# Performance work log

Measured on AMD Instinct MI355X. Metric: run time of the kernel, lower is better.

## Reference

```python
import jax, jax.numpy as jnp
import numpy as np

NF = 64      # feature channels of h
K = 3        # dynamic filter spatial size (padding=1 in source implies k=3)
FACTOR = 4   # pixel-unshuffle factor


def shuffle_down(x, f):
    # torch pixel_unshuffle: (B,C,H*f,W*f) -> (B,C*f*f,H,W)
    B, C, H, W = x.shape
    x = x.reshape(B, C, H // f, f, W // f, f)
    x = x.transpose(0, 1, 3, 5, 2, 4)
    return x.reshape(B, C * f * f, H // f, W // f)


def _patches3x3(x):
    # x: (B,C,H,W) -> (B,C,9,H,W): zero-padded 3x3 neighborhoods, row-major taps,
    # identical to the identity-filter grouped conv (im2col) in the source.
    H, W = x.shape[-2], x.shape[-1]
    xp = jnp.pad(x, ((0, 0), (0, 0), (1, 1), (1, 1)))
    shifts = [xp[:, :, dy:dy + H, dx:dx + W] for dy in range(K) for dx in range(K)]
    return jnp.stack(shifts, axis=2)


def setup_inputs() -> dict:
    key = jax.random.key(0)
    k1, k2, k3, k4 = jax.random.split(key, 4)
    B, H, W = 2, 256, 256
    h = jax.random.normal(k1, (B, NF, H, W), dtype=jnp.float32)
    i_t = jax.random.normal(k2, (B, 3, H * FACTOR, W * FACTOR), dtype=jnp.float32)
    conv_w = jax.random.normal(k3, (K * K, 3 * FACTOR ** 2, K, K), dtype=jnp.float32) * 0.05
    conv_b = jax.random.normal(k4, (K * K,), dtype=jnp.float32) * 0.05
    return {"h": h, "i_t": i_t, "conv_w": conv_w, "conv_b": conv_b}


def reference(h, i_t, conv_w, conv_b):
    # predict per-pixel 3x3 filters from the shuffled-down guidance frame
    x = shuffle_down(i_t, FACTOR)  # (B, 48, H, W)
    f = jax.lax.conv_general_dilated(
        x, conv_w, window_strides=(1, 1), padding=((1, 1), (1, 1)),
        dimension_numbers=("NCHW", "OIHW", "NCHW"))
    filters = jax.nn.relu(f + conv_b[None, :, None, None])  # (B, 9, H, W)

    # dynamic per-pixel conv: same 3x3 filter applied to every channel of h
    patches = _patches3x3(h)  # (B, nf, 9, H, W)
    out = jnp.einsum("bcfhw,bfhw->bchw", patches, filters)  # (B, nf, H, W)
    return out
```

## Files before the change

### kernel.cpp

```cpp
#include <hip/hip_runtime.h>

#define HSZ 256
#define WSZ 256
#define NFC 64
#define PLANE (HSZ * WSZ)

typedef __attribute__((ext_vector_type(8))) short short8;
typedef __attribute__((ext_vector_type(4))) float f32x4;

__device__ inline unsigned short f2bf(float f) {
    unsigned u = __builtin_bit_cast(unsigned, f);
    return (unsigned short)((u + 0x7fffu + ((u >> 16) & 1u)) >> 16);
}

__global__ __launch_bounds__(512, 4) void fused_dynfilter_v6(
    const float* __restrict__ hbuf,
    const float* __restrict__ i_t,
    const float* __restrict__ wbuf,
    const float* __restrict__ bias,
    float* __restrict__ out)
{
    __shared__ __align__(16) unsigned char smem[41856];
    unsigned short* const xs  = (unsigned short*)smem;
    unsigned short* const lwT = (unsigned short*)(smem + 32640);
    float* const lf = (float*)(smem + 32640);

    const int tid = threadIdx.x;

    const int lin = blockIdx.x + 8 * (blockIdx.y + 32 * blockIdx.z);
    const int q   = ((int)gridDim.z * 256) >> 3;
    const int nid = (lin & 7) * q + (lin >> 3);
    const int b   = nid >> 8;
    const int rem = nid & 255;
    const int X0  = (rem & 7) * 32;
    const int Y0  = (rem >> 3) * 8;

    const int lane = tid & 63;
    const int l15  = lane & 15;
    const int kg   = lane >> 4;
    const int wv   = tid >> 6;
    const int xh   = wv & 1;
    const int r0   = (wv >> 1) * 2;

    const float bv = (l15 < 9) ? bias[l15] : 0.f;
    const float* itb = i_t + (size_t)b * 3 * (PLANE * 16);

    {
        float4 lreg[8]; int sdst[8];
#pragma unroll
        for (int k = 0; k < 8; ++k) {
            const int v = tid + 512 * k;
            const int sp = v / 12, t = v - sp * 12;
            const int c3 = t >> 2, fy = t & 3;
            const int ly = sp / 34, lx = sp - ly * 34;
            const int Y = Y0 - 1 + ly, X = X0 - 1 + lx;
            float4 val = make_float4(0.f, 0.f, 0.f, 0.f);
            if (v < 4080 && (unsigned)Y < HSZ && (unsigned)X < WSZ)
                val = *(const float4*)(itb + ((size_t)c3 * 1024 + (4 * Y + fy)) * 1024 + 4 * X);
            lreg[k] = val;
            sdst[k] = (v < 4080) ? (sp * 48 + t * 4) : -1;
        }
#pragma unroll
        for (int k = 0; k < 8; ++k)
            if (sdst[k] >= 0) {
                ushort4 u{f2bf(lreg[k].x), f2bf(lreg[k].y), f2bf(lreg[k].z), f2bf(lreg[k].w)};
                *(ushort4*)(xs + sdst[k]) = u;
            }
    }

    {
        float4 wr[2];
#pragma unroll
        for (int k = 0; k < 2; ++k) {
            const int v = tid + 512 * k;
            wr[k] = (v < 972) ? *(const float4*)(wbuf + (size_t)v * 4)
                              : make_float4(0.f, 0.f, 0.f, 0.f);
        }
#pragma unroll
        for (int k = 0; k < 2; ++k) {
            const int v = tid + 512 * k;
            if (v < 972) {
                const float e[4] = {wr[k].x, wr[k].y, wr[k].z, wr[k].w};
#pragma unroll
                for (int j = 0; j < 4; ++j) {
                    const int n  = v * 4 + j;
                    const int oc = n / 432;
                    const int r  = n - 432 * oc;
                    const int ic = r / 9;
                    const int kk = r - 9 * ic;
                    lwT[oc * 432 + kk * 48 + ic] = f2bf(e[j]);
                }
            }
        }
    }

    __syncthreads();

    short8 wf[14];
    {
        const unsigned short* lwb = lwT + l15 * 432 + kg * 8;
#pragma unroll
        for (int kb = 0; kb < 14; ++kb) {
            short8 w = {0, 0, 0, 0, 0, 0, 0, 0};
            if (l15 < 9 && !(kb == 13 && kg >= 2))
                w = *(const short8*)(lwb + kb * 32);
            wf[kb] = w;
        }
    }

    f32x4 acc0 = {0.f, 0.f, 0.f, 0.f}, acc1 = acc0;
#pragma unroll
    for (int kb = 0; kb < 14; ++kb) {
        const int k0 = kb * 32 + kg * 8;
        int off = 0;
        if (k0 < 432) {
            const int kk = k0 / 48, ic0 = k0 - 48 * kk;
            const int ky = kk / 3, kx = kk - 3 * ky;
            off = ((r0 + ky) * 34 + 16 * xh + l15 + kx) * 48 + ic0;
        }
        short8 a0 = *(const short8*)(xs + off);
        short8 a1 = *(const short8*)(xs + off + 1632);
        acc0 = __builtin_amdgcn_mfma_f32_16x16x32_bf16(a0, wf[kb], acc0, 0, 0, 0);
        acc1 = __builtin_amdgcn_mfma_f32_16x16x32_bf16(a1, wf[kb], acc1, 0, 0, 0);
    }

    __syncthreads();

    const int pq  = tid & 7;
    const int py  = (tid >> 3) & 7;
    const int clo = tid >> 6;
    const int col0 = X0 + pq * 4;
    const bool gl = (col0 >= 4);
    const bool gr = (col0 <= WSZ - 8);

    bool rg[3]; int ro[3];
#pragma unroll
    for (int ky = 0; ky < 3; ++ky) {
        const int Y = Y0 + py - 1 + ky;
        rg[ky] = ((unsigned)Y < HSZ);
        ro[ky] = Y * WSZ + col0;
    }
    const float* hp = hbuf + ((size_t)b * NFC + clo * 8) * PLANE;

    float4 pf[9];
#pragma unroll
    for (int ky = 0; ky < 3; ++ky) {
        pf[ky * 3 + 0] = (rg[ky] && gl) ? *(const float4*)(hp + ro[ky] - 4)
                                        : make_float4(0.f, 0.f, 0.f, 0.f);
        pf[ky * 3 + 1] = rg[ky] ? *(const float4*)(hp + ro[ky])
                                : make_float4(0.f, 0.f, 0.f, 0.f);
        pf[ky * 3 + 2] = (rg[ky] && gr) ? *(const float4*)(hp + ro[ky] + 4)
                                        : make_float4(0.f, 0.f, 0.f, 0.f);
    }

    if (l15 < 9) {
#pragma unroll
        for (int t = 0; t < 2; ++t) {
            const int pyw = r0 + t;
            const f32x4 A = t ? acc1 : acc0;
#pragma unroll
            for (int r = 0; r < 4; ++r)
                lf[l15 * 256 + pyw * 32 + 16 * xh + kg * 4 + r] = fmaxf(A[r] + bv, 0.f);
        }
    }

    __syncthreads();

    float4 flt[9];
#pragma unroll
    for (int oc = 0; oc < 9; ++oc)
        flt[oc] = *(const float4*)(lf + oc * 256 + py * 32 + pq * 4);

    float* op = out + ((size_t)b * NFC + clo * 8) * PLANE
                    + (size_t)(Y0 + py) * WSZ + col0;

#pragma unroll
    for (int it = 0; it < 8; ++it) {
        const float* p = hp + (size_t)it * PLANE;

        float a[4] = {0.f, 0.f, 0.f, 0.f};
#pragma unroll
        for (int ky = 0; ky < 3; ++ky) {
            float4 lv, mv, rv;
            if (it == 0) {
                lv = pf[ky * 3 + 0]; mv = pf[ky * 3 + 1]; rv = pf[ky * 3 + 2];
            } else {
                lv = (rg[ky] && gl) ? *(const float4*)(p + ro[ky] - 4)
                                    : make_float4(0.f, 0.f, 0.f, 0.f);
                mv = rg[ky] ? *(const float4*)(p + ro[ky])
                            : make_float4(0.f, 0.f, 0.f, 0.f);
                rv = (rg[ky] && gr) ? *(const float4*)(p + ro[ky] + 4)
                                    : make_float4(0.f, 0.f, 0.f, 0.f);
            }
            const float vs[12] = {lv.x, lv.y, lv.z, lv.w,
                                  mv.x, mv.y, mv.z, mv.w,
                                  rv.x, rv.y, rv.z, rv.w};
#pragma unroll
            for (int kx = 0; kx < 3; ++kx)
#pragma unroll
                for (int j = 0; j < 4; ++j)
                    a[j] = fmaf(vs[3 + kx + j], flt[ky * 3 + kx][j], a[j]);
        }

        *(float4*)(op + (size_t)it * PLANE)
            = make_float4(a[0], a[1], a[2], a[3]);
    }
}

extern "C" void kernel_launch(void* const* d_in, const int* in_sizes, int n_in,
                              void* d_out, int out_size, void* d_ws, size_t ws_size,
                              hipStream_t stream) {
    const float* h      = (const float*)d_in[0];
    const float* i_t    = (const float*)d_in[1];
    const float* conv_w = (const float*)d_in[2];
    const float* conv_b = (const float*)d_in[3];
    float* out = (float*)d_out;

    const int B = in_sizes[0] / (NFC * PLANE);
    dim3 grid(8, 32, B);
    fused_dynfilter_v6<<<grid, 512, 0, stream>>>(h, i_t, conv_w, conv_b, out);
}
```

Before: 120.1 us.

## Double tile height, share horizontal halo via lane shuffles, prefetch next channel

Blocks grow to 1024 threads covering 16x32 output tiles, which halves the redundant guidance halo rows loaded per tile. In the dynamic-filter stage each thread now loads only its own float4 of h plus single edge scalars, and gets the left and right neighbours through wavefront shuffles instead of three float4 loads per row. The next channel's h values are software-prefetched into registers while the current one is computed, and one barrier is removed. Tradeoffs: about 85KB of LDS and 1024-thread blocks limit how many blocks fit per CU, and the extra shuffles and register pressure may cut occupancy.

```diff
diff --git a/kernel.cpp b/kernel.cpp
--- a/kernel.cpp
+++ b/kernel.cpp
@@ -13,34 +13,32 @@
     return (unsigned short)((u + 0x7fffu + ((u >> 16) & 1u)) >> 16);
 }
 
-__global__ __launch_bounds__(512, 4) void fused_dynfilter_v6(
+__global__ __launch_bounds__(1024, 4) void fused_dynfilter_v9(
     const float* __restrict__ hbuf,
     const float* __restrict__ i_t,
     const float* __restrict__ wbuf,
     const float* __restrict__ bias,
     float* __restrict__ out)
 {
-    __shared__ __align__(16) unsigned char smem[41856];
+    __shared__ __align__(16) unsigned char smem[84960];
     unsigned short* const xs  = (unsigned short*)smem;
-    unsigned short* const lwT = (unsigned short*)(smem + 32640);
-    float* const lf = (float*)(smem + 32640);
+    unsigned short* const lwT = (unsigned short*)(smem + 58752);
+    float* const lf = (float*)(smem + 66528);
 
     const int tid = threadIdx.x;
 
-    const int lin = blockIdx.x + 8 * (blockIdx.y + 32 * blockIdx.z);
-    const int q   = ((int)gridDim.z * 256) >> 3;
+    const int lin = blockIdx.x + 8 * (blockIdx.y + 16 * blockIdx.z);
+    const int q   = ((int)gridDim.z * 128) >> 3;
     const int nid = (lin & 7) * q + (lin >> 3);
-    const int b   = nid >> 8;
-    const int rem = nid & 255;
+    const int b   = nid >> 7;
+    const int rem = nid & 127;
     const int X0  = (rem & 7) * 32;
-    const int Y0  = (rem >> 3) * 8;
+    const int Y0  = (rem >> 3) * 16;
 
     const int lane = tid & 63;
     const int l15  = lane & 15;
     const int kg   = lane >> 4;
     const int wv   = tid >> 6;
-    const int xh   = wv & 1;
-    const int r0   = (wv >> 1) * 2;
 
     const float bv = (l15 < 9) ? bias[l15] : 0.f;
     const float* itb = i_t + (size_t)b * 3 * (PLANE * 16);
@@ -49,16 +47,16 @@
         float4 lreg[8]; int sdst[8];
 #pragma unroll
         for (int k = 0; k < 8; ++k) {
-            const int v = tid + 512 * k;
+            const int v = tid + 1024 * k;
             const int sp = v / 12, t = v - sp * 12;
             const int c3 = t >> 2, fy = t & 3;
             const int ly = sp / 34, lx = sp - ly * 34;
             const int Y = Y0 - 1 + ly, X = X0 - 1 + lx;
             float4 val = make_float4(0.f, 0.f, 0.f, 0.f);
-            if (v < 4080 && (unsigned)Y < HSZ && (unsigned)X < WSZ)
+            if (v < 7344 && (unsigned)Y < HSZ && (unsigned)X < WSZ)
                 val = *(const float4*)(itb + ((size_t)c3 * 1024 + (4 * Y + fy)) * 1024 + 4 * X);
             lreg[k] = val;
-            sdst[k] = (v < 4080) ? (sp * 48 + t * 4) : -1;
+            sdst[k] = (v < 7344) ? (sp * 48 + t * 4) : -1;
         }
 #pragma unroll
         for (int k = 0; k < 8; ++k)
@@ -69,27 +67,18 @@
     }
 
     {
-        float4 wr[2];
-#pragma unroll
-        for (int k = 0; k < 2; ++k) {
-            const int v = tid + 512 * k;
-            wr[k] = (v < 972) ? *(const float4*)(wbuf + (size_t)v * 4)
-                              : make_float4(0.f, 0.f, 0.f, 0.f);
-        }
-#pragma unroll
-        for (int k = 0; k < 2; ++k) {
-            const int v = tid + 512 * k;
-            if (v < 972) {
-                const float e[4] = {wr[k].x, wr[k].y, wr[k].z, wr[k].w};
-#pragma unroll
-                for (int j = 0; j < 4; ++j) {
-                    const int n  = v * 4 + j;
-                    const int oc = n / 432;
-                    const int r  = n - 432 * oc;
-                    const int ic = r / 9;
-                    const int kk = r - 9 * ic;
-                    lwT[oc * 432 + kk * 48 + ic] = f2bf(e[j]);
-                }
+        const int v = tid;
+        if (v < 972) {
+            float4 w4 = *(const float4*)(wbuf + (size_t)v * 4);
+            const float e[4] = {w4.x, w4.y, w4.z, w4.w};
+#pragma unroll
+            for (int j = 0; j < 4; ++j) {
+                const int n  = v * 4 + j;
+                const int oc = n / 432;
+                const int r  = n - 432 * oc;
+                const int ic = r / 9;
+                const int kk = r - 9 * ic;
+                lwT[oc * 432 + kk * 48 + ic] = f2bf(e[j]);
             }
         }
     }
@@ -116,22 +105,18 @@
         if (k0 < 432) {
             const int kk = k0 / 48, ic0 = k0 - 48 * kk;
             const int ky = kk / 3, kx = kk - 3 * ky;
-            off = ((r0 + ky) * 34 + 16 * xh + l15 + kx) * 48 + ic0;
+            off = ((wv + ky) * 34 + l15 + kx) * 48 + ic0;
         }
         short8 a0 = *(const short8*)(xs + off);
-        short8 a1 = *(const short8*)(xs + off + 1632);
+        short8 a1 = *(const short8*)(xs + off + 768);
         acc0 = __builtin_amdgcn_mfma_f32_16x16x32_bf16(a0, wf[kb], acc0, 0, 0, 0);
         acc1 = __builtin_amdgcn_mfma_f32_16x16x32_bf16(a1, wf[kb], acc1, 0, 0, 0);
     }
 
-    __syncthreads();
-
     const int pq  = tid & 7;
-    const int py  = (tid >> 3) & 7;
-    const int clo = tid >> 6;
+    const int py  = (tid >> 3) & 15;
+    const int clo = tid >> 7;
     const int col0 = X0 + pq * 4;
-    const bool gl = (col0 >= 4);
-    const bool gr = (col0 <= WSZ - 8);
 
     bool rg[3]; int ro[3];
 #pragma unroll
@@ -140,27 +125,25 @@
         rg[ky] = ((unsigned)Y < HSZ);
         ro[ky] = Y * WSZ + col0;
     }
+    const bool doL = (pq == 0) && (X0 > 0);
+    const bool doR = (pq == 7) && (X0 + 32 < WSZ);
     const float* hp = hbuf + ((size_t)b * NFC + clo * 8) * PLANE;
 
-    float4 pf[9];
+    float4 cm[3]; float cl[3], cr[3];
 #pragma unroll
     for (int ky = 0; ky < 3; ++ky) {
-        pf[ky * 3 + 0] = (rg[ky] && gl) ? *(const float4*)(hp + ro[ky] - 4)
-                                        : make_float4(0.f, 0.f, 0.f, 0.f);
-        pf[ky * 3 + 1] = rg[ky] ? *(const float4*)(hp + ro[ky])
-                                : make_float4(0.f, 0.f, 0.f, 0.f);
-        pf[ky * 3 + 2] = (rg[ky] && gr) ? *(const float4*)(hp + ro[ky] + 4)
-                                        : make_float4(0.f, 0.f, 0.f, 0.f);
+        cm[ky] = rg[ky] ? *(const float4*)(hp + ro[ky]) : make_float4(0.f, 0.f, 0.f, 0.f);
+        cl[ky] = (doL && rg[ky]) ? hp[ro[ky] - 1] : 0.f;
+        cr[ky] = (doR && rg[ky]) ? hp[ro[ky] + 4] : 0.f;
     }
 
     if (l15 < 9) {
 #pragma unroll
         for (int t = 0; t < 2; ++t) {
-            const int pyw = r0 + t;
             const f32x4 A = t ? acc1 : acc0;
 #pragma unroll
             for (int r = 0; r < 4; ++r)
-                lf[l15 * 256 + pyw * 32 + 16 * xh + kg * 4 + r] = fmaxf(A[r] + bv, 0.f);
+                lf[l15 * 512 + wv * 32 + t * 16 + kg * 4 + r] = fmaxf(A[r] + bv, 0.f);
         }
     }
 
@@ -169,41 +152,49 @@
     float4 flt[9];
 #pragma unroll
     for (int oc = 0; oc < 9; ++oc)
-        flt[oc] = *(const float4*)(lf + oc * 256 + py * 32 + pq * 4);
+        flt[oc] = *(const float4*)(lf + oc * 512 + py * 32 + pq * 4);
 
     float* op = out + ((size_t)b * NFC + clo * 8) * PLANE
                     + (size_t)(Y0 + py) * WSZ + col0;
 
 #pragma unroll
     for (int it = 0; it < 8; ++it) {
-        const float* p = hp + (size_t)it * PLANE;
+        float4 nm[3]; float nl[3], nr[3];
+        if (it < 7) {
+            const float* pn = hp + (size_t)(it + 1) * PLANE;
+#pragma unroll
+            for (int ky = 0; ky < 3; ++ky) {
+                nm[ky] = rg[ky] ? *(const float4*)(pn + ro[ky]) : make_float4(0.f, 0.f, 0.f, 0.f);
+                nl[ky] = (doL && rg[ky]) ? pn[ro[ky] - 1] : 0.f;
+                nr[ky] = (doR && rg[ky]) ? pn[ro[ky] + 4] : 0.f;
+            }
+        }
 
         float a[4] = {0.f, 0.f, 0.f, 0.f};
 #pragma unroll
         for (int ky = 0; ky < 3; ++ky) {
-            float4 lv, mv, rv;
-            if (it == 0) {
-                lv = pf[ky * 3 + 0]; mv = pf[ky * 3 + 1]; rv = pf[ky * 3 + 2];
-            } else {
-                lv = (rg[ky] && gl) ? *(const float4*)(p + ro[ky] - 4)
-                                    : make_float4(0.f, 0.f, 0.f, 0.f);
-                mv = rg[ky] ? *(const float4*)(p + ro[ky])
-                            : make_float4(0.f, 0.f, 0.f, 0.f);
-                rv = (rg[ky] && gr) ? *(const float4*)(p + ro[ky] + 4)
-                                    : make_float4(0.f, 0.f, 0.f, 0.f);
-            }
-            const float vs[12] = {lv.x, lv.y, lv.z, lv.w,
-                                  mv.x, mv.y, mv.z, mv.w,
-                                  rv.x, rv.y, rv.z, rv.w};
+            const float4 w = cm[ky];
+            float lv = __shfl(w.w, lane - 1);
+            float rv = __shfl(w.x, lane + 1);
+            if (pq == 0) lv = cl[ky];
+            if (pq == 7) rv = cr[ky];
+            const float vs[6] = {lv, w.x, w.y, w.z, w.w, rv};
 #pragma unroll
             for (int kx = 0; kx < 3; ++kx)
 #pragma unroll
                 for (int j = 0; j < 4; ++j)
-                    a[j] = fmaf(vs[3 + kx + j], flt[ky * 3 + kx][j], a[j]);
+                    a[j] = fmaf(vs[kx + j], flt[ky * 3 + kx][j], a[j]);
         }
 
         *(float4*)(op + (size_t)it * PLANE)
             = make_float4(a[0], a[1], a[2], a[3]);
+
+        if (it < 7) {
+#pragma unroll
+            for (int ky = 0; ky < 3; ++ky) {
+                cm[ky] = nm[ky]; cl[ky] = nl[ky]; cr[ky] = nr[ky];
+            }
+        }
     }
 }
 
@@ -217,6 +208,6 @@
     float* out = (float*)d_out;
 
     const int B = in_sizes[0] / (NFC * PLANE);
-    dim3 grid(8, 32, B);
-    fused_dynfilter_v6<<<grid, 512, 0, stream>>>(h, i_t, conv_w, conv_b, out);
+    dim3 grid(8, 16, B);
+    fused_dynfilter_v9<<<grid, 1024, 0, stream>>>(h, i_t, conv_w, conv_b, out);
 }
```

New measurement: 117.6 us. 1.02x faster.
